# Performance work log

Hardware: AMD Instinct MI355X
Metric: run time of the kernel (lower is better)

Reference implementation:

```python
import jax, jax.numpy as jnp
import numpy as np
from jax.scipy.ndimage import map_coordinates

IMG = 256
N_ANG = 50
BATCH = 4
N_CNN = 32
IN_CH = 2


def _circle_mask(S):
    c = (S - 1) / 2.0
    yy, xx = jnp.meshgrid(jnp.arange(S, dtype=jnp.float32), jnp.arange(S, dtype=jnp.float32), indexing='ij')
    return (((yy - c) ** 2 + (xx - c) ** 2) <= (S / 2.0) ** 2).astype(jnp.float32)


def radon_forward(img, angles):
    # img [B,1,S,S] -> sinogram [B,1,A,S]; parallel-beam, clip_to_circle=True
    S = img.shape[-1]
    c = (S - 1) / 2.0
    img = img * _circle_mask(S)
    t = jnp.arange(S, dtype=jnp.float32) - c        # integration coord
    s = jnp.arange(S, dtype=jnp.float32) - c        # detector coord
    cos = jnp.cos(angles)[:, None, None]
    sin = jnp.sin(angles)[:, None, None]
    x = s[None, None, :] * cos - t[None, :, None] * sin   # [A,S,S]
    y = s[None, None, :] * sin + t[None, :, None] * cos
    coords = jnp.stack([y + c, x + c])                    # [2,A,S,S] (row, col)
    samp = jax.vmap(lambda im: map_coordinates(im, coords, order=1, mode='constant', cval=0.0))(img[:, 0])  # [B,A,S,S]
    return samp.sum(axis=2)[:, None]                      # sum over ray param -> [B,1,A,S]


def filter_sinogram(sino):
    # Ram-Lak FFT filter with zero-padding + FBP normalization
    S = sino.shape[-1]
    A = sino.shape[2]
    P = max(64, int(2 ** np.ceil(np.log2(2 * S))))
    f = jnp.fft.rfft(jnp.pad(sino, ((0, 0), (0, 0), (0, 0), (0, P - S))), axis=-1)
    ramp = 2.0 * jnp.fft.rfftfreq(P).astype(jnp.float32)
    out = jnp.fft.irfft(f * ramp, n=P, axis=-1)[..., :S]
    return out * (np.pi / (2.0 * A))


def radon_backprojection(sino, angles):
    # sino [B,1,A,S] -> image [B,1,S,S]
    B, _, A, S = sino.shape
    c = (S - 1) / 2.0
    yy, xx = jnp.meshgrid(jnp.arange(S, dtype=jnp.float32) - c, jnp.arange(S, dtype=jnp.float32) - c, indexing='ij')
    cos = jnp.cos(angles)[:, None, None]
    sin = jnp.sin(angles)[:, None, None]
    det = xx[None] * cos + yy[None] * sin + c             # [A,S,S] detector coord
    sino2 = sino[:, 0]                                    # [B,A,S]

    def interp_one(sino_a, idx):
        # sino_a [B,S], idx [S,S] -> [B,S,S] linear interp, zero outside
        i0 = jnp.clip(jnp.floor(idx).astype(jnp.int32), 0, S - 2)
        w = idx - i0
        v = sino_a[:, i0] * (1.0 - w) + sino_a[:, i0 + 1] * w
        valid = (idx >= 0.0) & (idx <= S - 1.0)
        return jnp.where(valid, v, 0.0)

    bp = jax.vmap(interp_one, in_axes=(1, 0))(sino2, det).sum(axis=0)  # [B,S,S]
    return (bp * _circle_mask(S))[:, None]


def conv2d(x, w, b):
    y = jax.lax.conv_general_dilated(x, w, (1, 1), 'SAME', dimension_numbers=('NCHW', 'OIHW', 'NCHW'))
    return y + b[None, :, None, None]


def setup_inputs() -> dict:
    key = jax.random.key(0)
    ks = jax.random.split(key, 10)
    angles = jnp.asarray(np.linspace(0, np.pi, N_ANG, endpoint=False), dtype=jnp.float32)
    return {
        'x_sinogram': jax.random.normal(ks[0], (BATCH, 1, N_ANG, IMG), dtype=jnp.float32),
        'y_img_prev': jax.random.normal(ks[1], (BATCH, 1, IMG, IMG), dtype=jnp.float32),
        'y_img_concat_prev': jax.random.normal(ks[2], (BATCH, 1, IMG, IMG), dtype=jnp.float32),
        'angles': angles,
        'step': jnp.float32(1.0),
        'w1': jax.random.normal(ks[3], (N_CNN, IN_CH, 3, 3), dtype=jnp.float32) * 0.1,
        'b1': jnp.zeros((N_CNN,), dtype=jnp.float32),
        'w2': jax.random.normal(ks[4], (N_CNN, N_CNN, 3, 3), dtype=jnp.float32) * 0.1,
        'b2': jnp.zeros((N_CNN,), dtype=jnp.float32),
        'w3': jax.random.normal(ks[5], (1, N_CNN, 3, 3), dtype=jnp.float32) * 0.1,
        'b3': jnp.zeros((1,), dtype=jnp.float32),
    }


def reference(x_sinogram, y_img_prev, y_img_concat_prev, angles, step, w1, b1, w2, b2, w3, b3):
    Ay = radon_forward(y_img_prev, angles)                 # [B,1,A,S]
    diff = Ay - x_sinogram
    filt = filter_sinogram(diff)
    fbp = radon_backprojection(filt, angles)               # [B,1,S,S]
    y_img_update = y_img_prev + step * fbp
    y_cat = jnp.concatenate([y_img_update, y_img_concat_prev], axis=1)  # [B,2,S,S]
    h = jax.nn.relu(conv2d(y_cat, w1, b1))
    h = jax.nn.relu(conv2d(h, w2, b2))
    y_img = conv2d(h, w3, b3)
    return (y_img, y_img_update)
```

## Files before the change

### kernel.cpp

```cpp
#include <hip/hip_runtime.h>
#include <math.h>

#define IMGS 256
#define NANG 50
#define BATCH 4
#define NCNN 32
#define PIX (IMGS*IMGS)
#define NPIX (BATCH*PIX)

#define PROW 258
#define PPIX (PROW*PROW)
#define PB   (PPIX*NCNN)

#define OFF_FILT  0
#define OFF_W2BF  51200
#define OFF_H1P   55808

static constexpr double PI_D = 3.14159265358979323846;

typedef unsigned short u16;
typedef unsigned int   u32;
typedef unsigned long long u64;
typedef __bf16 bfrag __attribute__((ext_vector_type(8)));
typedef float  ffrag __attribute__((ext_vector_type(4)));

__device__ __forceinline__ u16 f2bf(float f) {
    u32 u = __float_as_uint(f);
    u += 0x7fffu + ((u >> 16) & 1u);
    return (u16)(u >> 16);
}

#define RPITCH_D 131
__global__ __launch_bounds__(512) void k_A(const float* __restrict__ angles,
                                           const float* __restrict__ yprev,
                                           const float* __restrict__ xsino,
                                           const float* __restrict__ w2,
                                           float* __restrict__ ws) {
    __shared__ u16 limg[258 * 262];
    __shared__ float spart[512];
    __shared__ float staps[512];
    __shared__ float srow[256];
    int tid = threadIdx.x;
    int gid = blockIdx.x;
    if (gid >= 200) {
        int i = (gid - 200) * 512 + tid;
        if (i < 9216) {
            int t = i >> 10, oc = (i >> 5) & 31, ic = i & 31;
            ((u16*)(ws + OFF_W2BF))[i] = f2bf(w2[(oc * 32 + ic) * 9 + t]);
        }
        return;
    }
    u32* l32 = (u32*)limg;
    int ra = gid;
    int a = ra % NANG, b = ra / NANG;

    if (tid < 511) {
        int d = tid - 255;
        int n = d < 0 ? -d : d;
        double g;
        if (n == 0) {
            g = 0.5;
        } else {
            double th = PI_D * (double)n / 256.0;
            double S = (256.0 * cos(255.0 * th) - 255.0 * cos(256.0 * th) - 1.0)
                       / (2.0 * (1.0 - cos(th)));
            double sign = (n & 1) ? -1.0 : 1.0;
            g = (sign + S / 128.0) / 512.0;
        }
        staps[tid] = (float)(g * PI_D / 100.0);
    }

    for (int z = tid; z < 772; z += 512) {
        int addr;
        if (z < 258)      addr = z * RPITCH_D;
        else if (z < 516) addr = (z - 258) * RPITCH_D + 129;
        else if (z < 644) addr = (z - 516) + 1;
        else              addr = 257 * RPITCH_D + (z - 644) + 1;
        l32[addr] = 0;
    }
    const float* __restrict__ src = yprev + b * PIX;
    for (int idx = tid; idx < 16384; idx += 512) {
        int r = idx >> 6, c4 = (idx & 63) << 2;
        float4 v = *(const float4*)(src + r * 256 + c4);
        float di = (float)r - 127.5f;
        float rr = di * di;
        float d0 = (float)c4 - 127.5f;
        v.x = (rr + d0 * d0 <= 16384.0f) ? v.x : 0.0f;
        v.y = (rr + (d0 + 1.0f) * (d0 + 1.0f) <= 16384.0f) ? v.y : 0.0f;
        v.z = (rr + (d0 + 2.0f) * (d0 + 2.0f) <= 16384.0f) ? v.z : 0.0f;
        v.w = (rr + (d0 + 3.0f) * (d0 + 3.0f) <= 16384.0f) ? v.w : 0.0f;
        u32 p0 = (u32)f2bf(v.x) | ((u32)f2bf(v.y) << 16);
        u32 p1 = (u32)f2bf(v.z) | ((u32)f2bf(v.w) << 16);
        int dw = (r + 1) * RPITCH_D + (c4 >> 1) + 1;
        l32[dw] = p0; l32[dw + 1] = p1;
    }
    __syncthreads();

    float a_ = angles[a];
    float cs = cosf(a_), sn = sinf(a_);
    int s = tid & 255, half = tid >> 8;
    float sc = (float)s - 127.5f;
    float t0c = 128.0f * (float)half - 127.5f;
    float rowv = sc * sn + t0c * cs + 127.5f;
    float colv = sc * cs - t0c * sn + 127.5f;
    float acc = 0.0f;
    #pragma unroll 4
    for (int it = 0; it < 128; ++it) {
        float fr = floorf(rowv), fc = floorf(colv);
        float wr = rowv - fr, wc = colv - fc;
        int i0 = (int)fr, j0 = (int)fc;
        bool valid = (rowv > -1.0f) & (rowv < 256.0f) & (colv > -1.0f) & (colv < 256.0f);
        int i0c = min(max(i0, -1), 255);
        int j0c = min(max(j0, -1), 255);
        int ca = j0c + 2;
        int ka = ca >> 1;
        int sh = (ca & 1) << 4;
        int dw = (i0c + 1) * RPITCH_D + ka;
        u32 A = l32[dw],            C = l32[dw + 1];
        u32 B = l32[dw + RPITCH_D], D = l32[dw + RPITCH_D + 1];
        u32 top = (u32)((((u64)C << 32) | (u64)A) >> sh);
        u32 bot = (u32)((((u64)D << 32) | (u64)B) >> sh);
        float tl = __uint_as_float(top << 16);
        float tr_ = __uint_as_float(top & 0xffff0000u);
        float bl = __uint_as_float(bot << 16);
        float br = __uint_as_float(bot & 0xffff0000u);
        float tv = tl + (tr_ - tl) * wc;
        float bv = bl + (br - bl) * wc;
        float sv = tv + (bv - tv) * wr;
        acc += valid ? sv : 0.0f;
        rowv += cs; colv -= sn;
    }
    spart[tid] = acc;
    __syncthreads();
    if (tid < 256)
        srow[tid] = spart[tid] + spart[tid + 256] - xsino[ra * 256 + tid];
    __syncthreads();
    {
        float fa = 0.0f;
        int m0 = half * 128;
        #pragma unroll 8
        for (int m = m0; m < m0 + 128; ++m) fa += srow[m] * staps[s - m + 255];
        spart[tid] = fa;
    }
    __syncthreads();
    if (tid < 256)
        ws[OFF_FILT + ra * 256 + tid] = spart[tid] + spart[tid + 256];
}

__global__ __launch_bounds__(512) void k_B(const float* __restrict__ angles,
                                           const float* __restrict__ yprev,
                                           const float* __restrict__ yconc,
                                           const float* __restrict__ stepp,
                                           const float* __restrict__ w1,
                                           const float* __restrict__ b1,
                                           float* __restrict__ ws,
                                           float* __restrict__ dout) {
    __shared__ float sf[NANG * 256];
    __shared__ float supd[6][258];
    __shared__ float scs[NANG], ssn[NANG];
    int tid = threadIdx.x;
    int b = blockIdx.x >> 6, tile = blockIdx.x & 63;
    int y0 = tile << 2;

    for (int idx = tid; idx < NANG * 256; idx += 512)
        sf[idx] = ws[OFF_FILT + b * (NANG * 256) + idx];
    if (tid < NANG) {
        float a_ = angles[tid];
        scs[tid] = cosf(a_); ssn[tid] = sinf(a_);
    }
    if (tid < 12) supd[tid >> 1][(tid & 1) * 257] = 0.0f;
    {
        int px_i0 = tile * 17;
        if (tid < 272) {
            int px_i = px_i0 + (tid >> 4), dw = tid & 15;
            if (px_i < 1028) {
                int y, x;
                if (px_i < 516) { y = (px_i < 258) ? 0 : 257; x = px_i % 258; }
                else            { int j = px_i - 516; y = 1 + (j >> 1); x = (j & 1) * 257; }
                u32* p = (u32*)((u16*)(ws + OFF_H1P) + b * PB + (y * PROW + x) * NCNN);
                p[dw] = 0;
            }
        }
    }
    __syncthreads();

    float step = stepp[0];
    for (int k = 0; k < 3; ++k) {
        int px = tid + k * 512;
        int r = px >> 8, j = px & 255;
        int iy = y0 - 1 + r;
        float val = 0.0f;
        if ((unsigned)iy < 256u) {
            float yy = (float)iy - 127.5f, xx = (float)j - 127.5f;
            float acc = 0.0f;
            #pragma unroll 5
            for (int a = 0; a < NANG; ++a) {
                float idxf = xx * scs[a] + yy * ssn[a] + 127.5f;
                float fl = floorf(idxf);
                int i0 = (int)fl;
                i0 = min(max(i0, 0), 254);
                float w = idxf - (float)i0;
                float v = sf[a * 256 + i0] * (1.0f - w) + sf[a * 256 + i0 + 1] * w;
                acc += (idxf >= 0.0f && idxf <= 255.0f) ? v : 0.0f;
            }
            float m = (xx * xx + yy * yy <= 16384.0f) ? 1.0f : 0.0f;
            val = yprev[b * PIX + iy * 256 + j] + step * acc * m;
            if (r >= 1 && r <= 4)
                dout[NPIX + b * PIX + iy * 256 + j] = val;
        }
        supd[r][j + 1] = val;
    }
    __syncthreads();

    for (int k = 0; k < 2; ++k) {
        int px = tid + k * 512;
        int rr = px >> 8, x = px & 255;
        int oy = y0 + rr;
        float v[18];
        #pragma unroll
        for (int ky = 0; ky < 3; ++ky)
            #pragma unroll
            for (int kx = 0; kx < 3; ++kx)
                v[ky * 3 + kx] = supd[rr + ky][x + kx];
        const float* __restrict__ in1 = yconc + b * PIX;
        #pragma unroll
        for (int ky = 0; ky < 3; ++ky)
            #pragma unroll
            for (int kx = 0; kx < 3; ++kx) {
                int yy = oy + ky - 1, xx = x + kx - 1;
                v[9 + ky * 3 + kx] =
                    ((unsigned)yy < 256u && (unsigned)xx < 256u) ? in1[yy * 256 + xx] : 0.0f;
            }
        u32 pk[16];
        #pragma unroll
        for (int oc2 = 0; oc2 < 16; ++oc2) {
            float a0 = b1[2 * oc2], a1 = b1[2 * oc2 + 1];
            const float* wp = w1 + (2 * oc2) * 18;
            #pragma unroll
            for (int t = 0; t < 18; ++t) { a0 += v[t] * wp[t]; a1 += v[t] * wp[18 + t]; }
            a0 = fmaxf(a0, 0.0f); a1 = fmaxf(a1, 0.0f);
            pk[oc2] = (u32)f2bf(a0) | ((u32)f2bf(a1) << 16);
        }
        uint4* o4 = (uint4*)((u16*)(ws + OFF_H1P) + b * PB + ((oy + 1) * PROW + (x + 1)) * NCNN);
        #pragma unroll
        for (int q = 0; q < 4; ++q)
            o4[q] = make_uint4(pk[4 * q], pk[4 * q + 1], pk[4 * q + 2], pk[4 * q + 3]);
    }
}

#define H2PITCH 34
__global__ __launch_bounds__(512) void k_C(const float* __restrict__ b2,
                                           const float* __restrict__ w3,
                                           const float* __restrict__ b3,
                                           float* __restrict__ ws,
                                           float* __restrict__ dout) {
    __shared__ u16 sh2[6 * 258 * H2PITCH];
    __shared__ float sw[288];
    u32* l32 = (u32*)sh2;
    int tid = threadIdx.x;
    int b = blockIdx.x >> 6, tile = blockIdx.x & 63;
    int y0 = tile << 2;

    for (int idx = tid; idx < 288; idx += 512)
        sw[idx] = w3[(idx & 31) * 9 + (idx >> 5)];
    for (int idx = tid; idx < 6 * 2 * 17; idx += 512) {
        int r = idx / 34, rem = idx % 34;
        int col = (rem < 17) ? 0 : 257, dw = rem % 17;
        l32[(r * 258 + col) * 17 + dw] = 0;
    }
    #pragma unroll
    for (int r = 0; r < 6; ++r) {
        int hy = y0 - 1 + r;
        if (hy < 0 || hy > 255)
            for (int idx = tid; idx < 258 * 17; idx += 512)
                l32[r * 258 * 17 + idx] = 0;
    }
    __syncthreads();

    const u16* __restrict__ w2bf = (const u16*)(ws + OFF_W2BF);
    const u16* __restrict__ h1b  = (const u16*)(ws + OFF_H1P) + b * PB;
    int wave = tid >> 6, lane = tid & 63;
    int m = lane & 15, quad = lane >> 4;
    bfrag Bf[9][2];
    #pragma unroll
    for (int t = 0; t < 9; ++t) {
        const u16* wp = w2bf + t * 1024 + m * 32 + quad * 8;
        Bf[t][0] = *(const bfrag*)(wp);
        Bf[t][1] = *(const bfrag*)(wp + 16 * 32);
    }
    float bias0 = b2[m], bias1 = b2[m + 16];
    #pragma unroll
    for (int k = 0; k < 12; ++k) {
        int tl = wave + (k << 3);
        int ridx = tl >> 4, xt = tl & 15;
        int hy = y0 - 1 + ridx;
        if ((unsigned)hy < 256u) {
            int xs = xt << 4;
            bfrag Af[9];
            #pragma unroll
            for (int t = 0; t < 9; ++t) {
                int ty = t / 3, tx = t % 3;
                const u16* ap = h1b + ((hy + ty) * PROW + xs + m + tx) * NCNN + quad * 8;
                Af[t] = *(const bfrag*)ap;
            }
            ffrag c0 = {0.f, 0.f, 0.f, 0.f}, c1 = {0.f, 0.f, 0.f, 0.f};
            #pragma unroll
            for (int t = 0; t < 9; ++t) {
                c0 = __builtin_amdgcn_mfma_f32_16x16x32_bf16(Af[t], Bf[t][0], c0, 0, 0, 0);
                c1 = __builtin_amdgcn_mfma_f32_16x16x32_bf16(Af[t], Bf[t][1], c1, 0, 0, 0);
            }
            #pragma unroll
            for (int r = 0; r < 4; ++r) {
                int px = xs + quad * 4 + r;
                u16* op = sh2 + (ridx * 258 + px + 1) * H2PITCH;
                op[m]      = f2bf(fmaxf(c0[r] + bias0, 0.0f));
                op[m + 16] = f2bf(fmaxf(c1[r] + bias1, 0.0f));
            }
        }
    }
    __syncthreads();

    {
        int pid = tid * 2;
        int rr = pid >> 8, x = pid & 255;
        int oy = y0 + rr;
        float bias = b3[0];
        float a0 = bias, a1 = bias;
        #pragma unroll
        for (int ky = 0; ky < 3; ++ky) {
            #pragma unroll
            for (int cx = 0; cx < 4; ++cx) {
                const u32* q = l32 + ((rr + ky) * 258 + x + cx) * 17;
                #pragma unroll
                for (int kd = 0; kd < 16; ++kd) {
                    u32 wv = q[kd];
                    float f0 = __uint_as_float(wv << 16);
                    float f1 = __uint_as_float(wv & 0xffff0000u);
                    int ch = kd * 2;
                    if (cx < 3) {
                        int t = ky * 3 + cx;
                        a0 += f0 * sw[t * 32 + ch] + f1 * sw[t * 32 + ch + 1];
                    }
                    if (cx > 0) {
                        int t = ky * 3 + cx - 1;
                        a1 += f0 * sw[t * 32 + ch] + f1 * sw[t * 32 + ch + 1];
                    }
                }
            }
        }
        float* op = dout + b * PIX + oy * 256 + x;
        op[0] = a0; op[1] = a1;
    }
}

extern "C" void kernel_launch(void* const* d_in, const int* in_sizes, int n_in,
                              void* d_out, int out_size, void* d_ws, size_t ws_size,
                              hipStream_t stream) {
    const float* xsino  = (const float*)d_in[0];
    const float* yprev  = (const float*)d_in[1];
    const float* yconc  = (const float*)d_in[2];
    const float* angles = (const float*)d_in[3];
    const float* stepp  = (const float*)d_in[4];
    const float* w1 = (const float*)d_in[5];
    const float* b1 = (const float*)d_in[6];
    const float* w2 = (const float*)d_in[7];
    const float* b2 = (const float*)d_in[8];
    const float* w3 = (const float*)d_in[9];
    const float* b3 = (const float*)d_in[10];
    float* out = (float*)d_out;
    float* ws  = (float*)d_ws;

    k_A<<<218, 512, 0, stream>>>(angles, yprev, xsino, w2, ws);
    k_B<<<BATCH * 64, 512, 0, stream>>>(angles, yprev, yconc, stepp, w1, b1, ws, out);
    k_C<<<BATCH * 64, 512, 0, stream>>>(b2, w3, b3, ws, out);
}
```

Before: 172.4 us.

## Double block sizes and restructure backprojection, conv1 and conv3 loops

k_A and k_C now run 1024-thread blocks, so each thread handles a quarter-length ray and k_C computes one output pixel per thread with bf16-packed conv3 weights. k_B stages the concat image in shared memory, reuses per-angle trig across three rows per thread, and gives each wave four conv1 output channels held in registers. k_C computes MFMA tiles without branching by clamping row indices and guarding only the store. The aim is more latency hiding and fewer redundant loads and branches. The cost is higher register pressure, and conv3 weights are now rounded to bf16.

```diff
diff --git a/kernel.cpp b/kernel.cpp
--- a/kernel.cpp
+++ b/kernel.cpp
@@ -31,19 +31,19 @@
 }
 
 #define RPITCH_D 131
-__global__ __launch_bounds__(512) void k_A(const float* __restrict__ angles,
-                                           const float* __restrict__ yprev,
-                                           const float* __restrict__ xsino,
-                                           const float* __restrict__ w2,
-                                           float* __restrict__ ws) {
+__global__ __launch_bounds__(1024) void k_A(const float* __restrict__ angles,
+                                            const float* __restrict__ yprev,
+                                            const float* __restrict__ xsino,
+                                            const float* __restrict__ w2,
+                                            float* __restrict__ ws) {
     __shared__ u16 limg[258 * 262];
-    __shared__ float spart[512];
+    __shared__ float spart[1024];
     __shared__ float staps[512];
     __shared__ float srow[256];
     int tid = threadIdx.x;
     int gid = blockIdx.x;
     if (gid >= 200) {
-        int i = (gid - 200) * 512 + tid;
+        int i = (gid - 200) * 1024 + tid;
         if (i < 9216) {
             int t = i >> 10, oc = (i >> 5) & 31, ic = i & 31;
             ((u16*)(ws + OFF_W2BF))[i] = f2bf(w2[(oc * 32 + ic) * 9 + t]);
@@ -70,7 +70,7 @@
         staps[tid] = (float)(g * PI_D / 100.0);
     }
 
-    for (int z = tid; z < 772; z += 512) {
+    for (int z = tid; z < 772; z += 1024) {
         int addr;
         if (z < 258)      addr = z * RPITCH_D;
         else if (z < 516) addr = (z - 258) * RPITCH_D + 129;
@@ -79,7 +79,7 @@
         l32[addr] = 0;
     }
     const float* __restrict__ src = yprev + b * PIX;
-    for (int idx = tid; idx < 16384; idx += 512) {
+    for (int idx = tid; idx < 16384; idx += 1024) {
         int r = idx >> 6, c4 = (idx & 63) << 2;
         float4 v = *(const float4*)(src + r * 256 + c4);
         float di = (float)r - 127.5f;
@@ -98,14 +98,14 @@
 
     float a_ = angles[a];
     float cs = cosf(a_), sn = sinf(a_);
-    int s = tid & 255, half = tid >> 8;
+    int s = tid & 255, q = tid >> 8;
     float sc = (float)s - 127.5f;
-    float t0c = 128.0f * (float)half - 127.5f;
+    float t0c = 64.0f * (float)q - 127.5f;
     float rowv = sc * sn + t0c * cs + 127.5f;
     float colv = sc * cs - t0c * sn + 127.5f;
     float acc = 0.0f;
     #pragma unroll 4
-    for (int it = 0; it < 128; ++it) {
+    for (int it = 0; it < 64; ++it) {
         float fr = floorf(rowv), fc = floorf(colv);
         float wr = rowv - fr, wc = colv - fc;
         int i0 = (int)fr, j0 = (int)fc;
@@ -133,30 +133,33 @@
     spart[tid] = acc;
     __syncthreads();
     if (tid < 256)
-        srow[tid] = spart[tid] + spart[tid + 256] - xsino[ra * 256 + tid];
+        srow[tid] = spart[tid] + spart[tid + 256] + spart[tid + 512] + spart[tid + 768]
+                    - xsino[ra * 256 + tid];
     __syncthreads();
     {
         float fa = 0.0f;
-        int m0 = half * 128;
+        int m0 = q * 64;
         #pragma unroll 8
-        for (int m = m0; m < m0 + 128; ++m) fa += srow[m] * staps[s - m + 255];
+        for (int m = m0; m < m0 + 64; ++m) fa += srow[m] * staps[s - m + 255];
         spart[tid] = fa;
     }
     __syncthreads();
     if (tid < 256)
-        ws[OFF_FILT + ra * 256 + tid] = spart[tid] + spart[tid + 256];
+        ws[OFF_FILT + ra * 256 + tid] =
+            spart[tid] + spart[tid + 256] + spart[tid + 512] + spart[tid + 768];
 }
 
-__global__ __launch_bounds__(512) void k_B(const float* __restrict__ angles,
-                                           const float* __restrict__ yprev,
-                                           const float* __restrict__ yconc,
-                                           const float* __restrict__ stepp,
-                                           const float* __restrict__ w1,
-                                           const float* __restrict__ b1,
-                                           float* __restrict__ ws,
-                                           float* __restrict__ dout) {
+__global__ __launch_bounds__(512, 4) void k_B(const float* __restrict__ angles,
+                                              const float* __restrict__ yprev,
+                                              const float* __restrict__ yconc,
+                                              const float* __restrict__ stepp,
+                                              const float* __restrict__ w1,
+                                              const float* __restrict__ b1,
+                                              float* __restrict__ ws,
+                                              float* __restrict__ dout) {
     __shared__ float sf[NANG * 256];
     __shared__ float supd[6][258];
+    __shared__ float sy2[6][258];
     __shared__ float scs[NANG], ssn[NANG];
     int tid = threadIdx.x;
     int b = blockIdx.x >> 6, tile = blockIdx.x & 63;
@@ -169,10 +172,15 @@
         scs[tid] = cosf(a_); ssn[tid] = sinf(a_);
     }
     if (tid < 12) supd[tid >> 1][(tid & 1) * 257] = 0.0f;
+    for (int idx = tid; idx < 6 * 258; idx += 512) {
+        int r = idx / 258, x = idx % 258;
+        int iy = y0 - 1 + r, ix = x - 1;
+        sy2[r][x] = ((unsigned)iy < 256u && (unsigned)ix < 256u)
+                        ? yconc[b * PIX + iy * 256 + ix] : 0.0f;
+    }
     {
-        int px_i0 = tile * 17;
         if (tid < 272) {
-            int px_i = px_i0 + (tid >> 4), dw = tid & 15;
+            int px_i = tile * 17 + (tid >> 4), dw = tid & 15;
             if (px_i < 1028) {
                 int y, x;
                 if (px_i < 516) { y = (px_i < 258) ? 0 : 257; x = px_i % 258; }
@@ -185,86 +193,99 @@
     __syncthreads();
 
     float step = stepp[0];
-    for (int k = 0; k < 3; ++k) {
-        int px = tid + k * 512;
-        int r = px >> 8, j = px & 255;
-        int iy = y0 - 1 + r;
-        float val = 0.0f;
-        if ((unsigned)iy < 256u) {
-            float yy = (float)iy - 127.5f, xx = (float)j - 127.5f;
-            float acc = 0.0f;
-            #pragma unroll 5
-            for (int a = 0; a < NANG; ++a) {
-                float idxf = xx * scs[a] + yy * ssn[a] + 127.5f;
-                float fl = floorf(idxf);
+    {
+        int j = tid & 255, r0 = tid >> 8;
+        float xx = (float)j - 127.5f;
+        float yy0 = (float)(y0 - 1 + r0) - 127.5f;
+        float acc[3] = {0.0f, 0.0f, 0.0f};
+        for (int a = 0; a < NANG; ++a) {
+            float cs = scs[a], sn = ssn[a];
+            float sn2 = sn + sn;
+            float f0 = xx * cs + yy0 * sn + 127.5f;
+            float idxf[3] = {f0, f0 + sn2, f0 + sn2 + sn2};
+            #pragma unroll
+            for (int k = 0; k < 3; ++k) {
+                float fl = floorf(idxf[k]);
                 int i0 = (int)fl;
                 i0 = min(max(i0, 0), 254);
-                float w = idxf - (float)i0;
+                float w = idxf[k] - (float)i0;
                 float v = sf[a * 256 + i0] * (1.0f - w) + sf[a * 256 + i0 + 1] * w;
-                acc += (idxf >= 0.0f && idxf <= 255.0f) ? v : 0.0f;
-            }
-            float m = (xx * xx + yy * yy <= 16384.0f) ? 1.0f : 0.0f;
-            val = yprev[b * PIX + iy * 256 + j] + step * acc * m;
-            if (r >= 1 && r <= 4)
-                dout[NPIX + b * PIX + iy * 256 + j] = val;
-        }
-        supd[r][j + 1] = val;
-    }
-    __syncthreads();
-
-    for (int k = 0; k < 2; ++k) {
-        int px = tid + k * 512;
-        int rr = px >> 8, x = px & 255;
-        int oy = y0 + rr;
-        float v[18];
-        #pragma unroll
-        for (int ky = 0; ky < 3; ++ky)
-            #pragma unroll
-            for (int kx = 0; kx < 3; ++kx)
-                v[ky * 3 + kx] = supd[rr + ky][x + kx];
-        const float* __restrict__ in1 = yconc + b * PIX;
-        #pragma unroll
-        for (int ky = 0; ky < 3; ++ky)
-            #pragma unroll
-            for (int kx = 0; kx < 3; ++kx) {
-                int yy = oy + ky - 1, xx = x + kx - 1;
-                v[9 + ky * 3 + kx] =
-                    ((unsigned)yy < 256u && (unsigned)xx < 256u) ? in1[yy * 256 + xx] : 0.0f;
-            }
-        u32 pk[16];
-        #pragma unroll
-        for (int oc2 = 0; oc2 < 16; ++oc2) {
-            float a0 = b1[2 * oc2], a1 = b1[2 * oc2 + 1];
-            const float* wp = w1 + (2 * oc2) * 18;
-            #pragma unroll
-            for (int t = 0; t < 18; ++t) { a0 += v[t] * wp[t]; a1 += v[t] * wp[18 + t]; }
-            a0 = fmaxf(a0, 0.0f); a1 = fmaxf(a1, 0.0f);
-            pk[oc2] = (u32)f2bf(a0) | ((u32)f2bf(a1) << 16);
-        }
-        uint4* o4 = (uint4*)((u16*)(ws + OFF_H1P) + b * PB + ((oy + 1) * PROW + (x + 1)) * NCNN);
-        #pragma unroll
-        for (int q = 0; q < 4; ++q)
-            o4[q] = make_uint4(pk[4 * q], pk[4 * q + 1], pk[4 * q + 2], pk[4 * q + 3]);
+                acc[k] += (idxf[k] >= 0.0f && idxf[k] <= 255.0f) ? v : 0.0f;
+            }
+        }
+        #pragma unroll
+        for (int k = 0; k < 3; ++k) {
+            int r = r0 + 2 * k;
+            int iy = y0 - 1 + r;
+            float val = 0.0f;
+            if ((unsigned)iy < 256u) {
+                float yy = (float)iy - 127.5f;
+                float m = (xx * xx + yy * yy <= 16384.0f) ? 1.0f : 0.0f;
+                val = yprev[b * PIX + iy * 256 + j] + step * acc[k] * m;
+                if (r >= 1 && r <= 4)
+                    dout[NPIX + b * PIX + iy * 256 + j] = val;
+            }
+            supd[r][j + 1] = val;
+        }
+    }
+    __syncthreads();
+
+    {
+        int wave = tid >> 6, lane = tid & 63;
+        int oc0 = wave * 4;
+        float W[72];
+        const float4* wsrc = (const float4*)(w1 + oc0 * 18);
+        #pragma unroll
+        for (int i = 0; i < 18; ++i) ((float4*)W)[i] = wsrc[i];
+        float bb0 = b1[oc0], bb1 = b1[oc0 + 1], bb2 = b1[oc0 + 2], bb3 = b1[oc0 + 3];
+        u16* h1base = (u16*)(ws + OFF_H1P) + b * PB;
+        for (int it = 0; it < 16; ++it) {
+            int px = it * 64 + lane;
+            int rr = px >> 8, x = px & 255;
+            int oy = y0 + rr;
+            float v[18];
+            #pragma unroll
+            for (int ky = 0; ky < 3; ++ky)
+                #pragma unroll
+                for (int kx = 0; kx < 3; ++kx) {
+                    v[ky * 3 + kx]     = supd[rr + ky][x + kx];
+                    v[9 + ky * 3 + kx] = sy2[rr + ky][x + kx];
+                }
+            float a0 = bb0, a1 = bb1, a2 = bb2, a3 = bb3;
+            #pragma unroll
+            for (int t = 0; t < 18; ++t) {
+                a0 += v[t] * W[t];
+                a1 += v[t] * W[18 + t];
+                a2 += v[t] * W[36 + t];
+                a3 += v[t] * W[54 + t];
+            }
+            u32 p0 = (u32)f2bf(fmaxf(a0, 0.0f)) | ((u32)f2bf(fmaxf(a1, 0.0f)) << 16);
+            u32 p1 = (u32)f2bf(fmaxf(a2, 0.0f)) | ((u32)f2bf(fmaxf(a3, 0.0f)) << 16);
+            u32* op = (u32*)(h1base + ((oy + 1) * PROW + (x + 1)) * NCNN + oc0);
+            op[0] = p0; op[1] = p1;
+        }
     }
 }
 
 #define H2PITCH 34
-__global__ __launch_bounds__(512) void k_C(const float* __restrict__ b2,
-                                           const float* __restrict__ w3,
-                                           const float* __restrict__ b3,
-                                           float* __restrict__ ws,
-                                           float* __restrict__ dout) {
+__global__ __launch_bounds__(1024) void k_C(const float* __restrict__ b2,
+                                            const float* __restrict__ w3,
+                                            const float* __restrict__ b3,
+                                            float* __restrict__ ws,
+                                            float* __restrict__ dout) {
     __shared__ u16 sh2[6 * 258 * H2PITCH];
-    __shared__ float sw[288];
+    __shared__ u32 swp[9 * 16];
     u32* l32 = (u32*)sh2;
     int tid = threadIdx.x;
     int b = blockIdx.x >> 6, tile = blockIdx.x & 63;
     int y0 = tile << 2;
 
-    for (int idx = tid; idx < 288; idx += 512)
-        sw[idx] = w3[(idx & 31) * 9 + (idx >> 5)];
-    for (int idx = tid; idx < 6 * 2 * 17; idx += 512) {
-        int r = idx / 34, rem = idx % 34;
+    if (tid < 144) {
+        int t = tid >> 4, kd = tid & 15;
+        swp[tid] = (u32)f2bf(w3[(2 * kd) * 9 + t]) | ((u32)f2bf(w3[(2 * kd + 1) * 9 + t]) << 16);
+    }
+    if (tid < 204) {
+        int r = tid / 34, rem = tid % 34;
         int col = (rem < 17) ? 0 : 257, dw = rem % 17;
         l32[(r * 258 + col) * 17 + dw] = 0;
     }
@@ -272,7 +293,7 @@
     for (int r = 0; r < 6; ++r) {
         int hy = y0 - 1 + r;
         if (hy < 0 || hy > 255)
-            for (int idx = tid; idx < 258 * 17; idx += 512)
+            for (int idx = tid; idx < 258 * 17; idx += 1024)
                 l32[r * 258 * 17 + idx] = 0;
     }
     __syncthreads();
@@ -290,25 +311,30 @@
     }
     float bias0 = b2[m], bias1 = b2[m + 16];
     #pragma unroll
-    for (int k = 0; k < 12; ++k) {
-        int tl = wave + (k << 3);
+    for (int k = 0; k < 6; ++k) {
+        int tl = wave + (k << 4);
         int ridx = tl >> 4, xt = tl & 15;
         int hy = y0 - 1 + ridx;
-        if ((unsigned)hy < 256u) {
-            int xs = xt << 4;
-            bfrag Af[9];
-            #pragma unroll
-            for (int t = 0; t < 9; ++t) {
+        bool valid = (unsigned)hy < 256u;
+        int hyc = min(max(hy, 0), 255);
+        int xs = xt << 4;
+        ffrag c0 = {0.f, 0.f, 0.f, 0.f}, c1 = {0.f, 0.f, 0.f, 0.f};
+        #pragma unroll
+        for (int g = 0; g < 3; ++g) {
+            bfrag Af[3];
+            #pragma unroll
+            for (int tt = 0; tt < 3; ++tt) {
+                int t = g * 3 + tt;
                 int ty = t / 3, tx = t % 3;
-                const u16* ap = h1b + ((hy + ty) * PROW + xs + m + tx) * NCNN + quad * 8;
-                Af[t] = *(const bfrag*)ap;
-            }
-            ffrag c0 = {0.f, 0.f, 0.f, 0.f}, c1 = {0.f, 0.f, 0.f, 0.f};
-            #pragma unroll
-            for (int t = 0; t < 9; ++t) {
-                c0 = __builtin_amdgcn_mfma_f32_16x16x32_bf16(Af[t], Bf[t][0], c0, 0, 0, 0);
-                c1 = __builtin_amdgcn_mfma_f32_16x16x32_bf16(Af[t], Bf[t][1], c1, 0, 0, 0);
-            }
+                Af[tt] = *(const bfrag*)(h1b + ((hyc + ty) * PROW + xs + m + tx) * NCNN + quad * 8);
+            }
+            #pragma unroll
+            for (int tt = 0; tt < 3; ++tt) {
+                c0 = __builtin_amdgcn_mfma_f32_16x16x32_bf16(Af[tt], Bf[g * 3 + tt][0], c0, 0, 0, 0);
+                c1 = __builtin_amdgcn_mfma_f32_16x16x32_bf16(Af[tt], Bf[g * 3 + tt][1], c1, 0, 0, 0);
+            }
+        }
+        if (valid) {
             #pragma unroll
             for (int r = 0; r < 4; ++r) {
                 int px = xs + quad * 4 + r;
@@ -321,35 +347,36 @@
     __syncthreads();
 
     {
-        int pid = tid * 2;
-        int rr = pid >> 8, x = pid & 255;
+        uint4 WP[9];
+        #pragma unroll
+        for (int t = 0; t < 9; ++t) WP[t] = ((const uint4*)swp)[t * 4 + 0],
+                                    WP[t] = *(const uint4*)(swp + t * 16);
+        u32 Wd[36];
+        #pragma unroll
+        for (int i = 0; i < 36; ++i) Wd[i] = swp[(i / 4) * 16 + (i & 3)];
+        (void)WP;
+        int rr = tid >> 8, x = tid & 255;
         int oy = y0 + rr;
-        float bias = b3[0];
-        float a0 = bias, a1 = bias;
+        float acc = b3[0];
         #pragma unroll
         for (int ky = 0; ky < 3; ++ky) {
             #pragma unroll
-            for (int cx = 0; cx < 4; ++cx) {
+            for (int cx = 0; cx < 3; ++cx) {
+                int t = ky * 3 + cx;
                 const u32* q = l32 + ((rr + ky) * 258 + x + cx) * 17;
                 #pragma unroll
                 for (int kd = 0; kd < 16; ++kd) {
-                    u32 wv = q[kd];
-                    float f0 = __uint_as_float(wv << 16);
-                    float f1 = __uint_as_float(wv & 0xffff0000u);
-                    int ch = kd * 2;
-                    if (cx < 3) {
-                        int t = ky * 3 + cx;
-                        a0 += f0 * sw[t * 32 + ch] + f1 * sw[t * 32 + ch + 1];
-                    }
-                    if (cx > 0) {
-                        int t = ky * 3 + cx - 1;
-                        a1 += f0 * sw[t * 32 + ch] + f1 * sw[t * 32 + ch + 1];
-                    }
+                    u32 hv = q[kd];
+                    u32 wv = (kd < 4) ? Wd[t * 4 + kd] : swp[t * 16 + kd];
+                    float h0 = __uint_as_float(hv << 16);
+                    float h1 = __uint_as_float(hv & 0xffff0000u);
+                    float w0 = __uint_as_float(wv << 16);
+                    float w1_ = __uint_as_float(wv & 0xffff0000u);
+                    acc += h0 * w0 + h1 * w1_;
                 }
             }
         }
-        float* op = dout + b * PIX + oy * 256 + x;
-        op[0] = a0; op[1] = a1;
+        dout[b * PIX + oy * 256 + x] = acc;
     }
 }
 
@@ -370,7 +397,7 @@
     float* out = (float*)d_out;
     float* ws  = (float*)d_ws;
 
-    k_A<<<218, 512, 0, stream>>>(angles, yprev, xsino, w2, ws);
+    k_A<<<209, 1024, 0, stream>>>(angles, yprev, xsino, w2, ws);
     k_B<<<BATCH * 64, 512, 0, stream>>>(angles, yprev, yconc, stepp, w1, b1, ws, out);
-    k_C<<<BATCH * 64, 512, 0, stream>>>(b2, w3, b3, ws, out);
+    k_C<<<BATCH * 64, 1024, 0, stream>>>(b2, w3, b3, ws, out);
 }
```

After: 157.6 us. 8.6% less time.
